# Kernel optimization log

Hardware: AMD Instinct MI355X
Metric: run time of the kernel (lower is better)

## Reference

```python
import jax, jax.numpy as jnp
import numpy as np

DIM = 1024
HEADS = 16
DIM_HEAD = 64
INNER = HEADS * DIM_HEAD  # 1024
SCALE = DIM_HEAD ** -0.5


def setup_inputs() -> dict:
    key = jax.random.key(0)
    k1, k2, k3, k4 = jax.random.split(key, 4)
    B, N = 2, 2048
    x = jax.random.normal(k1, (B, N, DIM), dtype=jnp.float32)
    # to_qkv: Linear(dim, 3*inner_dim, bias=False); weight stored as [out, in] in torch,
    # here as [in, out] for x @ W.
    w_qkv = jax.random.normal(k2, (DIM, 3 * INNER), dtype=jnp.float32) * (DIM ** -0.5)
    # to_out: Linear(inner_dim, dim) with bias
    w_out = jax.random.normal(k3, (INNER, DIM), dtype=jnp.float32) * (INNER ** -0.5)
    b_out = jax.random.normal(k4, (DIM,), dtype=jnp.float32) * 0.02
    return {"x": x, "w_qkv": w_qkv, "w_out": w_out, "b_out": b_out}


def reference(x, w_qkv, w_out, b_out):
    B, N, _ = x.shape
    qkv = x @ w_qkv                                  # [B, N, 3*INNER]
    q, k, v = jnp.split(qkv, 3, axis=-1)             # each [B, N, INNER]
    def to_heads(t):
        return t.reshape(B, N, HEADS, DIM_HEAD).transpose(0, 2, 1, 3)  # [B,H,N,D]
    q, k, v = to_heads(q), to_heads(k), to_heads(v)
    dots = jnp.einsum('bhnd,bhmd->bhnm', q, k) * SCALE  # [B,H,N,N]
    attn = jax.nn.softmax(dots, axis=-1)
    out = jnp.einsum('bhnm,bhmd->bhnd', attn, v)        # [B,H,N,D]
    out = out.transpose(0, 2, 1, 3).reshape(B, N, INNER)
    return out @ w_out + b_out
```

## Files before the change

kernel.cpp:

```cpp
#include <hip/hip_runtime.h>
#include <hip/hip_bf16.h>
#include <stdint.h>

#define PDIM   1024
#define HEADS  16
#define DHEAD  64
#define BATCH  2
#define SEQ    2048
#define ROWS   (BATCH*SEQ)
#define NBH    (BATCH*HEADS)

typedef __attribute__((ext_vector_type(8))) short s8v;
typedef __attribute__((ext_vector_type(4))) float f32x4;
typedef unsigned short ushort_t;
typedef unsigned int   uint32;

#define QSCALE 0.18033688011112042f
#define MFIX 12.0f

__device__ __forceinline__ ushort_t f2bf(float x){
  union { float f; uint32 u; } v; v.f = x;
  uint32 r = v.u + 0x7FFFu + ((v.u >> 16) & 1u);
  return (ushort_t)(r >> 16);
}
__device__ __forceinline__ float bf2f(ushort_t h){
  union { float f; uint32 u; } v; v.u = ((uint32)h) << 16;
  return v.f;
}

typedef const __attribute__((address_space(1))) void* gas_ptr;
typedef __attribute__((address_space(3))) void*       las_ptr;
__device__ __forceinline__ void g2l16(const void* g, void* l){
  __builtin_amdgcn_global_load_lds((gas_ptr)g, (las_ptr)l, 16, 0, 0);
}

__global__ __launch_bounds__(256) void k_cvt(const float* __restrict__ src,
                                             ushort_t* __restrict__ dst, int n4){
  int i = blockIdx.x * 256 + threadIdx.x;
  if (i >= n4) return;
  float4 v = reinterpret_cast<const float4*>(src)[i];
  reinterpret_cast<ushort4*>(dst)[i] =
      make_ushort4(f2bf(v.x), f2bf(v.y), f2bf(v.z), f2bf(v.w));
}

__global__ __launch_bounds__(256) void k_tcvt(const float* __restrict__ src, int R, int C,
                                              ushort_t* __restrict__ dh){
  __shared__ float tile[64][65];
  int cb = blockIdx.x * 64, rb = blockIdx.y * 64;
  int t = threadIdx.x;
  int lw = t >> 6;
  int lc = t & 63;
#pragma unroll
  for (int i = 0; i < 16; i++){
    int r = i * 4 + lw;
    tile[r][lc] = src[(size_t)(rb + r) * C + cb + lc];
  }
  __syncthreads();
#pragma unroll
  for (int i = 0; i < 16; i++){
    int c = i * 4 + lw;
    dh[(size_t)(cb + c) * R + rb + lc] = f2bf(tile[lc][c]);
  }
}

#define GBM 128
#define GBN 128
#define GBK 64

__global__ __launch_bounds__(256, 2) void k_gemm_qkv(
    const ushort_t* __restrict__ Xh, const ushort_t* __restrict__ Wqt_h,
    ushort_t* __restrict__ Qh, ushort_t* __restrict__ Ql,
    ushort_t* __restrict__ Kh, ushort_t* __restrict__ Vth){
  __shared__ __align__(16) ushort_t Asm[2][GBM * GBK];
  __shared__ __align__(16) ushort_t Bsm[2][GBM * GBK];
  const int tid  = threadIdx.x;
  const int wave = tid >> 6, lane = tid & 63;
  const int mb = blockIdx.y * GBM, nb = blockIdx.x * GBN;
  const int wr = wave >> 1, wc = wave & 1;
  const int l15 = lane & 15, l4 = lane >> 4;
  const int rsub = lane >> 3;
  const int schunk = ((lane & 7) ^ rsub) * 8;
  f32x4 acc[4][4] = {};

  auto stage = [&](int buf, int kb){
    int k0 = kb * GBK;
#pragma unroll
    for (int i = 0; i < 4; i++){
      int row = (i * 4 + wave) * 8 + rsub;
      g2l16(Xh    + (size_t)(mb + row) * 1024 + k0 + schunk, &Asm[buf][(i * 4 + wave) * 512]);
      g2l16(Wqt_h + (size_t)(nb + row) * 1024 + k0 + schunk, &Bsm[buf][(i * 4 + wave) * 512]);
    }
  };

  stage(0, 0);

  for (int kb = 0; kb < 16; kb++){
    const int cur = kb & 1;
    if (kb < 15){
      stage(cur ^ 1, kb + 1);
      asm volatile("s_waitcnt vmcnt(8)" ::: "memory");
    } else {
      asm volatile("s_waitcnt vmcnt(0)" ::: "memory");
    }
    __builtin_amdgcn_s_barrier();
    __builtin_amdgcn_s_setprio(1);
#pragma unroll
    for (int ks = 0; ks < 2; ks++){
      s8v af[4], bfr[4];
#pragma unroll
      for (int f = 0; f < 4; f++){
        int ch = (((ks * 4 + l4) ^ (l15 & 7)) << 3);
        af[f]  = *reinterpret_cast<const s8v*>(&Asm[cur][(wr * 64 + f * 16 + l15) * 64 + ch]);
        bfr[f] = *reinterpret_cast<const s8v*>(&Bsm[cur][(wc * 64 + f * 16 + l15) * 64 + ch]);
      }
#pragma unroll
      for (int fr = 0; fr < 4; fr++)
#pragma unroll
        for (int fc = 0; fc < 4; fc++)
          acc[fr][fc] = __builtin_amdgcn_mfma_f32_16x16x32_bf16(af[fr], bfr[fc], acc[fr][fc], 0, 0, 0);
    }
    __builtin_amdgcn_s_setprio(0);
    __builtin_amdgcn_s_barrier();
  }

  const int pnum = nb >> 10;
#pragma unroll
  for (int fr = 0; fr < 4; fr++){
    int row  = mb + wr * 64 + fr * 16 + l4 * 4;
    int b    = row >> 11;
    int nseq = row & 2047;
#pragma unroll
    for (int fc = 0; fc < 4; fc++){
      int col = nb + wc * 64 + fc * 16 + l15;
      int rem = col & 1023;
      int h = rem >> 6, d = rem & 63;
      int bh = b * 16 + h;
      if (pnum == 0){
        size_t base = ((size_t)bh * SEQ + nseq) * 64 + d;
#pragma unroll
        for (int r = 0; r < 4; r++){
          float q = acc[fr][fc][r] * QSCALE;
          ushort_t qh_ = f2bf(q);
          Qh[base + (size_t)r * 64] = qh_;
          Ql[base + (size_t)r * 64] = f2bf(q - bf2f(qh_));
        }
      } else if (pnum == 1){
        size_t base = ((size_t)bh * SEQ + nseq) * 64 + d;
#pragma unroll
        for (int r = 0; r < 4; r++)
          Kh[base + (size_t)r * 64] = f2bf(acc[fr][fc][r]);
      } else {
        size_t base = ((size_t)bh * 64 + d) * SEQ + nseq;
        *reinterpret_cast<ushort4*>(&Vth[base]) =
            make_ushort4(f2bf(acc[fr][fc][0]), f2bf(acc[fr][fc][1]),
                         f2bf(acc[fr][fc][2]), f2bf(acc[fr][fc][3]));
      }
    }
  }
}

__global__ __launch_bounds__(256, 2) void k_gemm_out(
    const ushort_t* __restrict__ Ah, const ushort_t* __restrict__ Bth,
    float* __restrict__ C, const float* __restrict__ bias){
  __shared__ __align__(16) ushort_t Asm[2][GBM * GBK];
  __shared__ __align__(16) ushort_t Bsm[2][GBM * GBK];
  const int tid  = threadIdx.x;
  const int wave = tid >> 6, lane = tid & 63;
  const int mb = blockIdx.y * GBM, nb = blockIdx.x * GBN;
  const int wr = wave >> 1, wc = wave & 1;
  const int l15 = lane & 15, l4 = lane >> 4;
  const int rsub = lane >> 3;
  const int schunk = ((lane & 7) ^ rsub) * 8;
  f32x4 acc[4][4] = {};

  auto stage = [&](int buf, int kb){
    int k0 = kb * GBK;
#pragma unroll
    for (int i = 0; i < 4; i++){
      int row = (i * 4 + wave) * 8 + rsub;
      g2l16(Ah  + (size_t)(mb + row) * 1024 + k0 + schunk, &Asm[buf][(i * 4 + wave) * 512]);
      g2l16(Bth + (size_t)(nb + row) * 1024 + k0 + schunk, &Bsm[buf][(i * 4 + wave) * 512]);
    }
  };

  stage(0, 0);

  for (int kb = 0; kb < 16; kb++){
    const int cur = kb & 1;
    if (kb < 15){
      stage(cur ^ 1, kb + 1);
      asm volatile("s_waitcnt vmcnt(8)" ::: "memory");
    } else {
      asm volatile("s_waitcnt vmcnt(0)" ::: "memory");
    }
    __builtin_amdgcn_s_barrier();
    __builtin_amdgcn_s_setprio(1);
#pragma unroll
    for (int ks = 0; ks < 2; ks++){
      s8v af[4], bfr[4];
#pragma unroll
      for (int f = 0; f < 4; f++){
        int ch = (((ks * 4 + l4) ^ (l15 & 7)) << 3);
        af[f]  = *reinterpret_cast<const s8v*>(&Asm[cur][(wr * 64 + f * 16 + l15) * 64 + ch]);
        bfr[f] = *reinterpret_cast<const s8v*>(&Bsm[cur][(wc * 64 + f * 16 + l15) * 64 + ch]);
      }
#pragma unroll
      for (int fr = 0; fr < 4; fr++)
#pragma unroll
        for (int fc = 0; fc < 4; fc++)
          acc[fr][fc] = __builtin_amdgcn_mfma_f32_16x16x32_bf16(af[fr], bfr[fc], acc[fr][fc], 0, 0, 0);
    }
    __builtin_amdgcn_s_setprio(0);
    __builtin_amdgcn_s_barrier();
  }
#pragma unroll
  for (int fr = 0; fr < 4; fr++){
    int row = mb + wr * 64 + fr * 16 + l4 * 4;
#pragma unroll
    for (int fc = 0; fc < 4; fc++){
      int col = nb + wc * 64 + fc * 16 + l15;
      float bv = bias[col];
#pragma unroll
      for (int r = 0; r < 4; r++)
        C[(size_t)(row + r) * 1024 + col] = acc[fr][fc][r] + bv;
    }
  }
}

__global__ __launch_bounds__(256, 2) void k_flash(
    const ushort_t* __restrict__ Qh, const ushort_t* __restrict__ Ql,
    const ushort_t* __restrict__ Kh, const ushort_t* __restrict__ Vth,
    ushort_t* __restrict__ Ah){
  __shared__ __align__(16) ushort_t KhS[2][64 * 64];
  __shared__ __align__(16) ushort_t VhS[2][64 * 64];
  __shared__ __align__(16) ushort_t PhS[128 * 72];
  const int lid = blockIdx.x;
  const int xcd = lid & 7, g = lid >> 3;
  const int bh = xcd * 4 + (g & 3);
  const int qb = (g >> 2) * 128;
  const int tid = threadIdx.x, wave = tid >> 6, lane = tid & 63;
  const int l15 = lane & 15, l4 = lane >> 4;
  const int b = bh >> 4, h = bh & 15;
  const size_t hbase = (size_t)bh * SEQ * 64;
  const int rsub = lane >> 3;
  const int schunk = ((lane & 7) ^ rsub) * 8;

  s8v qhf[2][2], qlf[2][2];
#pragma unroll
  for (int fr = 0; fr < 2; fr++)
#pragma unroll
    for (int ks = 0; ks < 2; ks++){
      size_t off = hbase + (size_t)(qb + wave * 32 + fr * 16 + l15) * 64 + ks * 32 + l4 * 8;
      qhf[fr][ks] = *reinterpret_cast<const s8v*>(&Qh[off]);
      qlf[fr][ks] = *reinterpret_cast<const s8v*>(&Ql[off]);
    }

  f32x4 o[2][4] = {};
  float lsum[2][4] = {};

  auto stage = [&](int buf, int kt){
    int kvb = kt * 64;
#pragma unroll
    for (int i = 0; i < 2; i++){
      int row = (i * 4 + wave) * 8 + rsub;
      g2l16(Kh  + hbase + (size_t)(kvb + row) * 64 + schunk, &KhS[buf][(i * 4 + wave) * 512]);
      g2l16(Vth + ((size_t)bh * 64 + row) * SEQ + kvb + schunk, &VhS[buf][(i * 4 + wave) * 512]);
    }
  };

  stage(0, 0);

  for (int kt = 0; kt < 32; kt++){
    const int cur = kt & 1;
    if (kt < 31){
      stage(cur ^ 1, kt + 1);
      asm volatile("s_waitcnt vmcnt(4)" ::: "memory");
    } else {
      asm volatile("s_waitcnt vmcnt(0)" ::: "memory");
    }
    __builtin_amdgcn_s_barrier();

    f32x4 s[2][4] = {};
    __builtin_amdgcn_s_setprio(1);
#pragma unroll
    for (int ks = 0; ks < 2; ks++)
#pragma unroll
      for (int fc = 0; fc < 4; fc++){
        int rK = fc * 16 + l15;
        int ch = ((ks * 4 + l4) ^ (rK & 7)) << 3;
        s8v kh = *reinterpret_cast<const s8v*>(&KhS[cur][rK * 64 + ch]);
#pragma unroll
        for (int fr = 0; fr < 2; fr++){
          s[fr][fc] = __builtin_amdgcn_mfma_f32_16x16x32_bf16(qhf[fr][ks], kh, s[fr][fc], 0, 0, 0);
          s[fr][fc] = __builtin_amdgcn_mfma_f32_16x16x32_bf16(qlf[fr][ks], kh, s[fr][fc], 0, 0, 0);
        }
      }
    __builtin_amdgcn_s_setprio(0);

#pragma unroll
    for (int fr = 0; fr < 2; fr++)
#pragma unroll
      for (int fc = 0; fc < 4; fc++)
#pragma unroll
        for (int r = 0; r < 4; r++){
          float p = __builtin_amdgcn_exp2f(s[fr][fc][r] - MFIX);
          lsum[fr][r] += p;
          int prow = wave * 32 + fr * 16 + l4 * 4 + r;
          int col  = (fc * 16 + l15) ^ (((prow >> 2) & 3) << 3);
          PhS[prow * 72 + col] = f2bf(p);
        }

    __builtin_amdgcn_s_setprio(1);
#pragma unroll
    for (int c = 0; c < 2; c++){
      s8v pa[2];
#pragma unroll
      for (int fr = 0; fr < 2; fr++){
        int prow = wave * 32 + fr * 16 + l15;
        int u = (prow >> 2) & 3;
        pa[fr] = *reinterpret_cast<const s8v*>(&PhS[prow * 72 + (((c * 4 + l4) ^ u) << 3)]);
      }
#pragma unroll
      for (int fd = 0; fd < 4; fd++){
        int rV = fd * 16 + l15;
        int ch = ((c * 4 + l4) ^ (rV & 7)) << 3;
        s8v vh = *reinterpret_cast<const s8v*>(&VhS[cur][rV * 64 + ch]);
        o[0][fd] = __builtin_amdgcn_mfma_f32_16x16x32_bf16(pa[0], vh, o[0][fd], 0, 0, 0);
        o[1][fd] = __builtin_amdgcn_mfma_f32_16x16x32_bf16(pa[1], vh, o[1][fd], 0, 0, 0);
      }
    }
    __builtin_amdgcn_s_setprio(0);
    __builtin_amdgcn_s_barrier();
  }

#pragma unroll
  for (int fr = 0; fr < 2; fr++)
#pragma unroll
    for (int msk = 1; msk < 16; msk <<= 1)
#pragma unroll
      for (int r = 0; r < 4; r++)
        lsum[fr][r] += __shfl_xor(lsum[fr][r], msk);
#pragma unroll
  for (int fr = 0; fr < 2; fr++)
#pragma unroll
    for (int r = 0; r < 4; r++){
      float inv = 1.f / lsum[fr][r];
      int n = qb + wave * 32 + fr * 16 + l4 * 4 + r;
      size_t rowbase = (size_t)(b * SEQ + n) * 1024 + h * 64;
#pragma unroll
      for (int fd = 0; fd < 4; fd++)
        Ah[rowbase + fd * 16 + l15] = f2bf(o[fr][fd][r] * inv);
    }
}

extern "C" void kernel_launch(void* const* d_in, const int* in_sizes, int n_in,
                              void* d_out, int out_size, void* d_ws, size_t ws_size,
                              hipStream_t stream){
  const float* x     = (const float*)d_in[0];
  const float* w_qkv = (const float*)d_in[1];
  const float* w_out = (const float*)d_in[2];
  const float* b_out = (const float*)d_in[3];
  float* out = (float*)d_out;
  char* ws = (char*)d_ws;

  ushort_t* Xh    = (ushort_t*)(ws);
  ushort_t* Wqt_h = (ushort_t*)(ws + 8388608);
  ushort_t* Wot_h = (ushort_t*)(ws + 14680064);
  ushort_t* Qh    = (ushort_t*)(ws + 16777216);
  ushort_t* Ql    = (ushort_t*)(ws + 25165824);
  ushort_t* Kh    = (ushort_t*)(ws + 33554432);
  ushort_t* Vth   = (ushort_t*)(ws + 41943040);
  ushort_t* Ah    = (ushort_t*)(ws + 50331648);

  k_cvt<<<4096, 256, 0, stream>>>(x, Xh, ROWS * PDIM / 4);
  k_tcvt<<<dim3(48, 16), 256, 0, stream>>>(w_qkv, 1024, 3072, Wqt_h);
  k_tcvt<<<dim3(16, 16), 256, 0, stream>>>(w_out, 1024, 1024, Wot_h);
  k_gemm_qkv<<<dim3(24, 32), 256, 0, stream>>>(Xh, Wqt_h, Qh, Ql, Kh, Vth);
  k_flash<<<512, 256, 0, stream>>>(Qh, Ql, Kh, Vth, Ah);
  k_gemm_out<<<dim3(8, 32), 256, 0, stream>>>(Ah, Wot_h, out, b_out);
}
```

Measured before the change: 137.0 us.

## Drop Q hi/lo split, transpose S MFMA, pack P stores, merge prep kernels

Removes the split-bf16 Q (high+low) representation, halving the QK^T MFMA count and the Q loads and stores. Swaps the MFMA operand order so each lane holds a whole row of S, which allows packed bf16 conversion and 8-byte P stores into a new XOR-swizzled LDS layout and a cheaper row-sum reduction. Also merges the three conversion and transpose launches into one prep kernel. Dropping the Q low part lowers score precision, and with a fixed softmax offset and no running max this could affect accuracy.

```diff
diff --git a/kernel.cpp b/kernel.cpp
--- a/kernel.cpp
+++ b/kernel.cpp
@@ -23,9 +23,10 @@
   uint32 r = v.u + 0x7FFFu + ((v.u >> 16) & 1u);
   return (ushort_t)(r >> 16);
 }
-__device__ __forceinline__ float bf2f(ushort_t h){
-  union { float f; uint32 u; } v; v.u = ((uint32)h) << 16;
-  return v.f;
+__device__ __forceinline__ uint32 cvt_pk_bf16(float lo, float hi){
+  uint32 r;
+  asm("v_cvt_pk_bf16_f32 %0, %1, %2" : "=v"(r) : "v"(lo), "v"(hi));
+  return r;
 }
 
 typedef const __attribute__((address_space(1))) void* gas_ptr;
@@ -34,22 +35,30 @@
   __builtin_amdgcn_global_load_lds((gas_ptr)g, (las_ptr)l, 16, 0, 0);
 }
 
-__global__ __launch_bounds__(256) void k_cvt(const float* __restrict__ src,
-                                             ushort_t* __restrict__ dst, int n4){
-  int i = blockIdx.x * 256 + threadIdx.x;
-  if (i >= n4) return;
-  float4 v = reinterpret_cast<const float4*>(src)[i];
-  reinterpret_cast<ushort4*>(dst)[i] =
-      make_ushort4(f2bf(v.x), f2bf(v.y), f2bf(v.z), f2bf(v.w));
-}
-
-__global__ __launch_bounds__(256) void k_tcvt(const float* __restrict__ src, int R, int C,
-                                              ushort_t* __restrict__ dh){
+__global__ __launch_bounds__(256) void k_prep(
+    const float* __restrict__ x, const float* __restrict__ w_qkv,
+    const float* __restrict__ w_out,
+    ushort_t* __restrict__ Xh, ushort_t* __restrict__ Wqt_h,
+    ushort_t* __restrict__ Wot_h){
   __shared__ float tile[64][65];
-  int cb = blockIdx.x * 64, rb = blockIdx.y * 64;
+  const int bid = blockIdx.x;
+  if (bid < 4096){
+    int i = bid * 256 + threadIdx.x;
+    float4 v = reinterpret_cast<const float4*>(x)[i];
+    reinterpret_cast<ushort4*>(Xh)[i] =
+        make_ushort4(f2bf(v.x), f2bf(v.y), f2bf(v.z), f2bf(v.w));
+    return;
+  }
+  const float* src; ushort_t* dst; int R, C, cb, rb;
+  if (bid < 4864){
+    int t = bid - 4096; src = w_qkv; dst = Wqt_h; R = 1024; C = 3072;
+    cb = (t % 48) * 64; rb = (t / 48) * 64;
+  } else {
+    int t = bid - 4864; src = w_out; dst = Wot_h; R = 1024; C = 1024;
+    cb = (t % 16) * 64; rb = (t / 16) * 64;
+  }
   int t = threadIdx.x;
-  int lw = t >> 6;
-  int lc = t & 63;
+  int lw = t >> 6, lc = t & 63;
 #pragma unroll
   for (int i = 0; i < 16; i++){
     int r = i * 4 + lw;
@@ -59,7 +68,7 @@
 #pragma unroll
   for (int i = 0; i < 16; i++){
     int c = i * 4 + lw;
-    dh[(size_t)(cb + c) * R + rb + lc] = f2bf(tile[lc][c]);
+    dst[(size_t)(cb + c) * R + rb + lc] = f2bf(tile[lc][c]);
   }
 }
 
@@ -69,8 +78,7 @@
 
 __global__ __launch_bounds__(256, 2) void k_gemm_qkv(
     const ushort_t* __restrict__ Xh, const ushort_t* __restrict__ Wqt_h,
-    ushort_t* __restrict__ Qh, ushort_t* __restrict__ Ql,
-    ushort_t* __restrict__ Kh, ushort_t* __restrict__ Vth){
+    ushort_t* __restrict__ Qh, ushort_t* __restrict__ Kh, ushort_t* __restrict__ Vth){
   __shared__ __align__(16) ushort_t Asm[2][GBM * GBK];
   __shared__ __align__(16) ushort_t Bsm[2][GBM * GBK];
   const int tid  = threadIdx.x;
@@ -138,12 +146,8 @@
       if (pnum == 0){
         size_t base = ((size_t)bh * SEQ + nseq) * 64 + d;
 #pragma unroll
-        for (int r = 0; r < 4; r++){
-          float q = acc[fr][fc][r] * QSCALE;
-          ushort_t qh_ = f2bf(q);
-          Qh[base + (size_t)r * 64] = qh_;
-          Ql[base + (size_t)r * 64] = f2bf(q - bf2f(qh_));
-        }
+        for (int r = 0; r < 4; r++)
+          Qh[base + (size_t)r * 64] = f2bf(acc[fr][fc][r] * QSCALE);
       } else if (pnum == 1){
         size_t base = ((size_t)bh * SEQ + nseq) * 64 + d;
 #pragma unroll
@@ -228,12 +232,11 @@
 }
 
 __global__ __launch_bounds__(256, 2) void k_flash(
-    const ushort_t* __restrict__ Qh, const ushort_t* __restrict__ Ql,
-    const ushort_t* __restrict__ Kh, const ushort_t* __restrict__ Vth,
-    ushort_t* __restrict__ Ah){
+    const ushort_t* __restrict__ Qh, const ushort_t* __restrict__ Kh,
+    const ushort_t* __restrict__ Vth, ushort_t* __restrict__ Ah){
   __shared__ __align__(16) ushort_t KhS[2][64 * 64];
   __shared__ __align__(16) ushort_t VhS[2][64 * 64];
-  __shared__ __align__(16) ushort_t PhS[128 * 72];
+  __shared__ __align__(16) ushort_t PhS[128 * 64];
   const int lid = blockIdx.x;
   const int xcd = lid & 7, g = lid >> 3;
   const int bh = xcd * 4 + (g & 3);
@@ -245,18 +248,17 @@
   const int rsub = lane >> 3;
   const int schunk = ((lane & 7) ^ rsub) * 8;
 
-  s8v qhf[2][2], qlf[2][2];
+  s8v qhf[2][2];
 #pragma unroll
   for (int fr = 0; fr < 2; fr++)
 #pragma unroll
     for (int ks = 0; ks < 2; ks++){
       size_t off = hbase + (size_t)(qb + wave * 32 + fr * 16 + l15) * 64 + ks * 32 + l4 * 8;
       qhf[fr][ks] = *reinterpret_cast<const s8v*>(&Qh[off]);
-      qlf[fr][ks] = *reinterpret_cast<const s8v*>(&Ql[off]);
     }
 
   f32x4 o[2][4] = {};
-  float lsum[2][4] = {};
+  float lsum[2] = {0.f, 0.f};
 
   auto stage = [&](int buf, int kt){
     int kvb = kt * 64;
@@ -289,26 +291,30 @@
         int rK = fc * 16 + l15;
         int ch = ((ks * 4 + l4) ^ (rK & 7)) << 3;
         s8v kh = *reinterpret_cast<const s8v*>(&KhS[cur][rK * 64 + ch]);
-#pragma unroll
-        for (int fr = 0; fr < 2; fr++){
-          s[fr][fc] = __builtin_amdgcn_mfma_f32_16x16x32_bf16(qhf[fr][ks], kh, s[fr][fc], 0, 0, 0);
-          s[fr][fc] = __builtin_amdgcn_mfma_f32_16x16x32_bf16(qlf[fr][ks], kh, s[fr][fc], 0, 0, 0);
-        }
+        s[0][fc] = __builtin_amdgcn_mfma_f32_16x16x32_bf16(kh, qhf[0][ks], s[0][fc], 0, 0, 0);
+        s[1][fc] = __builtin_amdgcn_mfma_f32_16x16x32_bf16(kh, qhf[1][ks], s[1][fc], 0, 0, 0);
       }
     __builtin_amdgcn_s_setprio(0);
 
 #pragma unroll
-    for (int fr = 0; fr < 2; fr++)
-#pragma unroll
-      for (int fc = 0; fc < 4; fc++)
-#pragma unroll
-        for (int r = 0; r < 4; r++){
-          float p = __builtin_amdgcn_exp2f(s[fr][fc][r] - MFIX);
-          lsum[fr][r] += p;
-          int prow = wave * 32 + fr * 16 + l4 * 4 + r;
-          int col  = (fc * 16 + l15) ^ (((prow >> 2) & 3) << 3);
-          PhS[prow * 72 + col] = f2bf(p);
-        }
+    for (int fr = 0; fr < 2; fr++){
+      int q = wave * 32 + fr * 16 + l15;
+      int key = q & 7;
+      int base = q * 64;
+#pragma unroll
+      for (int fc = 0; fc < 4; fc++){
+        float p0 = __builtin_amdgcn_exp2f(s[fr][fc][0] - MFIX);
+        float p1 = __builtin_amdgcn_exp2f(s[fr][fc][1] - MFIX);
+        float p2 = __builtin_amdgcn_exp2f(s[fr][fc][2] - MFIX);
+        float p3 = __builtin_amdgcn_exp2f(s[fr][fc][3] - MFIX);
+        lsum[fr] += (p0 + p1) + (p2 + p3);
+        uint2 w;
+        w.x = cvt_pk_bf16(p0, p1);
+        w.y = cvt_pk_bf16(p2, p3);
+        *reinterpret_cast<uint2*>(
+            &PhS[base + (((2 * fc + (l4 >> 1)) ^ key) << 3) + ((l4 & 1) << 2)]) = w;
+      }
+    }
 
     __builtin_amdgcn_s_setprio(1);
 #pragma unroll
@@ -316,9 +322,8 @@
       s8v pa[2];
 #pragma unroll
       for (int fr = 0; fr < 2; fr++){
-        int prow = wave * 32 + fr * 16 + l15;
-        int u = (prow >> 2) & 3;
-        pa[fr] = *reinterpret_cast<const s8v*>(&PhS[prow * 72 + (((c * 4 + l4) ^ u) << 3)]);
+        int q = wave * 32 + fr * 16 + l15;
+        pa[fr] = *reinterpret_cast<const s8v*>(&PhS[q * 64 + (((c * 4 + l4) ^ (q & 7)) << 3)]);
       }
 #pragma unroll
       for (int fd = 0; fd < 4; fd++){
@@ -334,23 +339,19 @@
   }
 
 #pragma unroll
-  for (int fr = 0; fr < 2; fr++)
-#pragma unroll
-    for (int msk = 1; msk < 16; msk <<= 1)
-#pragma unroll
-      for (int r = 0; r < 4; r++)
-        lsum[fr][r] += __shfl_xor(lsum[fr][r], msk);
-#pragma unroll
-  for (int fr = 0; fr < 2; fr++)
+  for (int fr = 0; fr < 2; fr++){
+    lsum[fr] += __shfl_xor(lsum[fr], 16);
+    lsum[fr] += __shfl_xor(lsum[fr], 32);
 #pragma unroll
     for (int r = 0; r < 4; r++){
-      float inv = 1.f / lsum[fr][r];
+      float inv = 1.f / __shfl(lsum[fr], l4 * 4 + r);
       int n = qb + wave * 32 + fr * 16 + l4 * 4 + r;
       size_t rowbase = (size_t)(b * SEQ + n) * 1024 + h * 64;
 #pragma unroll
       for (int fd = 0; fd < 4; fd++)
         Ah[rowbase + fd * 16 + l15] = f2bf(o[fr][fd][r] * inv);
     }
+  }
 }
 
 extern "C" void kernel_launch(void* const* d_in, const int* in_sizes, int n_in,
@@ -367,15 +368,12 @@
   ushort_t* Wqt_h = (ushort_t*)(ws + 8388608);
   ushort_t* Wot_h = (ushort_t*)(ws + 14680064);
   ushort_t* Qh    = (ushort_t*)(ws + 16777216);
-  ushort_t* Ql    = (ushort_t*)(ws + 25165824);
-  ushort_t* Kh    = (ushort_t*)(ws + 33554432);
-  ushort_t* Vth   = (ushort_t*)(ws + 41943040);
-  ushort_t* Ah    = (ushort_t*)(ws + 50331648);
-
-  k_cvt<<<4096, 256, 0, stream>>>(x, Xh, ROWS * PDIM / 4);
-  k_tcvt<<<dim3(48, 16), 256, 0, stream>>>(w_qkv, 1024, 3072, Wqt_h);
-  k_tcvt<<<dim3(16, 16), 256, 0, stream>>>(w_out, 1024, 1024, Wot_h);
-  k_gemm_qkv<<<dim3(24, 32), 256, 0, stream>>>(Xh, Wqt_h, Qh, Ql, Kh, Vth);
-  k_flash<<<512, 256, 0, stream>>>(Qh, Ql, Kh, Vth, Ah);
+  ushort_t* Kh    = (ushort_t*)(ws + 25165824);
+  ushort_t* Vth   = (ushort_t*)(ws + 33554432);
+  ushort_t* Ah    = (ushort_t*)(ws + 41943040);
+
+  k_prep<<<5120, 256, 0, stream>>>(x, w_qkv, w_out, Xh, Wqt_h, Wot_h);
+  k_gemm_qkv<<<dim3(24, 32), 256, 0, stream>>>(Xh, Wqt_h, Qh, Kh, Vth);
+  k_flash<<<512, 256, 0, stream>>>(Qh, Kh, Vth, Ah);
   k_gemm_out<<<dim3(8, 32), 256, 0, stream>>>(Ah, Wot_h, out, b_out);
 }
```

Result: faster. 115.7 us (-15.6%).
